# Kernel tuning notes

Hardware: AMD Instinct MI355X
Metric: run time of the kernel (lower is better)

## Reference

```python
import jax, jax.numpy as jnp
import numpy as np

N = 100000
E = 800000
F_IN = 256
HID = 64
H = 4
NEG_SLOPE = 0.2
BN_EPS = 1e-5


def setup_inputs() -> dict:
    key = jax.random.key(0)
    ks = jax.random.split(key, 20)
    s = 0.05
    return {
        "x": jax.random.normal(ks[0], (N, F_IN), jnp.float32),
        "edge_index": jax.random.randint(ks[1], (2, E), 0, N, jnp.int64),
        # GCNConv params
        "W_gcn": jax.random.normal(ks[2], (F_IN, HID), jnp.float32) * s,
        "b_gcn": jnp.zeros((HID,), jnp.float32),
        "g0": jnp.ones((HID,), jnp.float32),
        "beta0": jnp.zeros((HID,), jnp.float32),
        # GATConv 1 params
        "W1": jax.random.normal(ks[3], (HID, H * HID), jnp.float32) * s,
        "a_src1": jax.random.normal(ks[4], (H, HID), jnp.float32) * s,
        "a_dst1": jax.random.normal(ks[5], (H, HID), jnp.float32) * s,
        "b1": jnp.zeros((H * HID,), jnp.float32),
        "g1": jnp.ones((H * HID,), jnp.float32),
        "beta1": jnp.zeros((H * HID,), jnp.float32),
        # GATConv 2 params
        "W2": jax.random.normal(ks[6], (H * HID, H * HID), jnp.float32) * s,
        "a_src2": jax.random.normal(ks[7], (H, HID), jnp.float32) * s,
        "a_dst2": jax.random.normal(ks[8], (H, HID), jnp.float32) * s,
        "b2": jnp.zeros((H * HID,), jnp.float32),
        "g2": jnp.ones((H * HID,), jnp.float32),
        "beta2": jnp.zeros((H * HID,), jnp.float32),
    }


def _add_self_loops(edge_index, n):
    loop = jnp.arange(n, dtype=edge_index.dtype)
    src = jnp.concatenate([edge_index[0], loop])
    dst = jnp.concatenate([edge_index[1], loop])
    return src, dst


def _batch_norm(x, g, b):
    # BatchNorm1d, training-mode batch stats (biased variance), no dropout
    m = x.mean(0)
    v = x.var(0)
    return g * (x - m) * jax.lax.rsqrt(v + BN_EPS) + b


def _gcn_conv(x, src, dst, W, b, n):
    # symmetric normalization with self-loops already included in src/dst
    deg = jax.ops.segment_sum(jnp.ones_like(dst, jnp.float32), dst, n)
    dinv = jax.lax.rsqrt(jnp.maximum(deg, 1.0))
    norm = dinv[src] * dinv[dst]  # [E']
    h = x @ W  # [N, HID]
    out = jax.ops.segment_sum(h[src] * norm[:, None], dst, n)
    return out + b


def _gat_conv(x, src, dst, W, a_src, a_dst, b, n):
    h = (x @ W).reshape(n, H, HID)  # [N, H, C]
    alpha_s = jnp.einsum("nhc,hc->nh", h, a_src)  # [N, H]
    alpha_d = jnp.einsum("nhc,hc->nh", h, a_dst)
    e = alpha_s[src] + alpha_d[dst]  # [E', H]
    e = jnp.where(e > 0, e, NEG_SLOPE * e)  # LeakyReLU
    # softmax over incoming edges of each dst node, per head
    emax = jax.ops.segment_max(e, dst, n)
    w = jnp.exp(e - emax[dst])
    wsum = jax.ops.segment_sum(w, dst, n)
    att = w / wsum[dst]  # [E', H]
    out = jax.ops.segment_sum(att[:, :, None] * h[src], dst, n)  # [N, H, C]
    return out.reshape(n, H * HID) + b


def reference(x, edge_index, W_gcn, b_gcn, g0, beta0, W1, a_src1, a_dst1, b1,
              g1, beta1, W2, a_src2, a_dst2, b2, g2, beta2):
    n = x.shape[0]
    src, dst = _add_self_loops(edge_index, n)
    h = jax.nn.relu(_gcn_conv(x, src, dst, W_gcn, b_gcn, n))
    h = _batch_norm(h, g0, beta0)
    h = _gat_conv(h, src, dst, W1, a_src1, a_dst1, b1, n)
    h = jax.nn.elu(_batch_norm(h, g1, beta1))
    h = _gat_conv(h, src, dst, W2, a_src2, a_dst2, b2, n)
    h = jax.nn.elu(_batch_norm(h, g2, beta2))
    return h
```

## Files before the change

kernel.cpp:

```cpp
#include <hip/hip_runtime.h>
#include <hip/hip_bf16.h>
#include <math.h>

#define NN 100000
#define EE 800000
#define FIN 256
#define CH 64
#define C1 256
#define BN_EPS 1e-5f
#define NEG_SLOPE 0.2f

typedef __attribute__((ext_vector_type(8))) short short8;
typedef __attribute__((ext_vector_type(8))) unsigned short u16x8;
typedef __attribute__((ext_vector_type(4))) float f32x4;

__device__ __forceinline__ float bf2f(ushort u) {
    return __uint_as_float(((unsigned)u) << 16);
}
__device__ __forceinline__ ushort f2bf(float f) {
    unsigned u = __float_as_uint(f);
    return (ushort)((u + 0x7FFF + ((u >> 16) & 1)) >> 16);
}

__global__ void hist_kernel(const int* __restrict__ ei, int* __restrict__ deg) {
    int t = blockIdx.x * 256 + threadIdx.x;
    if (t < EE) atomicAdd(&deg[ei[EE + t]], 1);
}
__global__ void dinv_kernel(const int* __restrict__ deg, float* __restrict__ dinv) {
    int i = blockIdx.x * 256 + threadIdx.x;
    if (i < NN) dinv[i] = rsqrtf((float)(deg[i] + 1));
}
__global__ void scan_k1(const int* __restrict__ deg, int* __restrict__ row_start,
                        int* __restrict__ bsum) {
    __shared__ int sh[256];
    int t = threadIdx.x;
    int i = blockIdx.x * 256 + t;
    int v = (i < NN) ? (deg[i] + 1) : 0;
    sh[t] = v;
    __syncthreads();
    for (int off = 1; off < 256; off <<= 1) {
        int add = (t >= off) ? sh[t - off] : 0;
        __syncthreads();
        sh[t] += add;
        __syncthreads();
    }
    if (i < NN) row_start[i] = sh[t] - v;
    if (t == 255) bsum[blockIdx.x] = sh[255];
}
__global__ void scan_k2(int* __restrict__ bsum, int nb) {
    __shared__ int sh[512];
    int t = threadIdx.x;
    int v = (t < nb) ? bsum[t] : 0;
    sh[t] = v;
    __syncthreads();
    for (int off = 1; off < 512; off <<= 1) {
        int add = (t >= off) ? sh[t - off] : 0;
        __syncthreads();
        sh[t] += add;
        __syncthreads();
    }
    if (t < nb) bsum[t] = sh[t] - v;
}
__global__ void scan_k3(int* __restrict__ row_start, const int* __restrict__ bsum) {
    int i = blockIdx.x * 256 + threadIdx.x;
    if (i < NN) row_start[i] += bsum[i >> 8];
    if (i == NN) row_start[NN] = EE + NN;
}
__global__ void scatter_kernel(const int* __restrict__ ei, const int* __restrict__ row_start,
                               int* __restrict__ fill, int* __restrict__ sorted) {
    int t = blockIdx.x * 256 + threadIdx.x;
    if (t >= EE + NN) return;
    int s, d;
    if (t < EE) { s = ei[t]; d = ei[EE + t]; }
    else        { s = t - EE; d = s; }
    int pos = atomicAdd(&fill[d], 1);
    sorted[row_start[d] + pos] = s;
}

__global__ void convert_f32_bf16(const float* __restrict__ in, ushort* __restrict__ out, long n4) {
    long i = (long)blockIdx.x * 256 + threadIdx.x;
    if (i < n4) {
        float4 v = *(const float4*)&in[i * 4];
        ushort4 o;
        o.x = f2bf(v.x); o.y = f2bf(v.y); o.z = f2bf(v.z); o.w = f2bf(v.w);
        *(ushort4*)&out[i * 4] = o;
    }
}
__global__ void transpose_w(const float* __restrict__ W, ushort* __restrict__ Bt, int M, int K) {
    int idx = blockIdx.x * 256 + threadIdx.x;
    if (idx < M * K) {
        int m = idx / K, n = idx % K;
        Bt[n * M + m] = f2bf(W[idx]);
    }
}

__global__ __launch_bounds__(256) void gemm_mfma(
        const ushort* __restrict__ A, const ushort* __restrict__ Bt,
        ushort* __restrict__ C, int M, int K) {
    __shared__ ushort As[64][40];
    __shared__ ushort Bs[64][40];
    int t = threadIdx.x;
    int w = t >> 6;
    int l = t & 63;
    int rowBase = blockIdx.y * 64;
    int colBase = blockIdx.x * 64;
    int srow = t >> 2;
    int sk = (t & 3) * 8;
    int m = l & 15, q = l >> 4;
    f32x4 acc[4] = {};
    for (int k0 = 0; k0 < M; k0 += 32) {
        uint4 av = make_uint4(0u, 0u, 0u, 0u);
        int gr = rowBase + srow;
        if (gr < NN) av = *(const uint4*)&A[(long)gr * M + k0 + sk];
        uint4 bv = *(const uint4*)&Bt[(long)(colBase + srow) * M + k0 + sk];
        *(uint4*)&As[srow][sk] = av;
        *(uint4*)&Bs[srow][sk] = bv;
        __syncthreads();
        short8 af = *(const short8*)&As[w * 16 + m][q * 8];
#pragma unroll
        for (int c = 0; c < 4; ++c) {
            short8 bf = *(const short8*)&Bs[c * 16 + m][q * 8];
            acc[c] = __builtin_amdgcn_mfma_f32_16x16x32_bf16(af, bf, acc[c], 0, 0, 0);
        }
        __syncthreads();
    }
#pragma unroll
    for (int c = 0; c < 4; ++c) {
#pragma unroll
        for (int r = 0; r < 4; ++r) {
            int orow = rowBase + w * 16 + q * 4 + r;
            if (orow < NN) C[(long)orow * K + colBase + c * 16 + m] = f2bf(acc[c][r]);
        }
    }
}

__global__ __launch_bounds__(256) void gcn_gather(
        const int* __restrict__ row_start, const int* __restrict__ sorted,
        const float* __restrict__ dinv, const ushort* __restrict__ h0,
        float* __restrict__ agg) {
    int node = blockIdx.x * 4 + (threadIdx.x >> 6);
    if (node >= NN) return;
    int l = threadIdx.x & 63;
    int slot = l >> 3;
    int li = l & 7;
    int c = li * 8;
    int b = row_start[node], e = row_start[node + 1];
    float a[8] = {};
    for (int i = b + slot; i < e; i += 8) {
        int s = sorted[i];
        float dv = dinv[s];
        u16x8 v = *(const u16x8*)&h0[(long)s * 64 + c];
#pragma unroll
        for (int j = 0; j < 8; ++j) a[j] += dv * bf2f((ushort)v[j]);
    }
#pragma unroll
    for (int j = 0; j < 8; ++j) {
        a[j] += __shfl_xor(a[j], 8);
        a[j] += __shfl_xor(a[j], 16);
        a[j] += __shfl_xor(a[j], 32);
    }
    if (slot == 0) {
        float dn = dinv[node];
        f32x4 o0, o1;
#pragma unroll
        for (int j = 0; j < 4; ++j) { o0[j] = a[j] * dn; o1[j] = a[4 + j] * dn; }
        *(f32x4*)&agg[(long)node * 64 + c] = o0;
        *(f32x4*)&agg[(long)node * 64 + c + 4] = o1;
    }
}

__global__ __launch_bounds__(256) void bn_stats64(
        const float* __restrict__ x, const float* __restrict__ bias,
        float* __restrict__ sums, float* __restrict__ sumsq) {
    __shared__ float red[4][16][8];
    int l = threadIdx.x & 63;
    int w = threadIdx.x >> 6;
    int wv = blockIdx.x * 4 + w;
    int nw = gridDim.x * 4;
    int sub = l >> 4;
    int c = (l & 15) * 4;
    f32x4 b4 = *(const f32x4*)&bias[c];
    float s0 = 0.f, s1 = 0.f, s2 = 0.f, s3 = 0.f;
    float q0 = 0.f, q1 = 0.f, q2 = 0.f, q3 = 0.f;
    for (int r = wv * 4 + sub; r < NN; r += nw * 4) {
        f32x4 v = *(const f32x4*)&x[(long)r * 64 + c];
        float v0 = fmaxf(v[0] + b4[0], 0.f);
        float v1 = fmaxf(v[1] + b4[1], 0.f);
        float v2 = fmaxf(v[2] + b4[2], 0.f);
        float v3 = fmaxf(v[3] + b4[3], 0.f);
        s0 += v0; s1 += v1; s2 += v2; s3 += v3;
        q0 += v0 * v0; q1 += v1 * v1; q2 += v2 * v2; q3 += v3 * v3;
    }
    s0 += __shfl_xor(s0, 16); s1 += __shfl_xor(s1, 16);
    s2 += __shfl_xor(s2, 16); s3 += __shfl_xor(s3, 16);
    q0 += __shfl_xor(q0, 16); q1 += __shfl_xor(q1, 16);
    q2 += __shfl_xor(q2, 16); q3 += __shfl_xor(q3, 16);
    s0 += __shfl_xor(s0, 32); s1 += __shfl_xor(s1, 32);
    s2 += __shfl_xor(s2, 32); s3 += __shfl_xor(s3, 32);
    q0 += __shfl_xor(q0, 32); q1 += __shfl_xor(q1, 32);
    q2 += __shfl_xor(q2, 32); q3 += __shfl_xor(q3, 32);
    if (sub == 0) {
        int li = l & 15;
        red[w][li][0] = s0; red[w][li][1] = s1; red[w][li][2] = s2; red[w][li][3] = s3;
        red[w][li][4] = q0; red[w][li][5] = q1; red[w][li][6] = q2; red[w][li][7] = q3;
    }
    __syncthreads();
    if (w == 0 && sub == 0) {
        int li = l & 15;
        atomicAdd(&sums[c + 0], red[0][li][0] + red[1][li][0] + red[2][li][0] + red[3][li][0]);
        atomicAdd(&sums[c + 1], red[0][li][1] + red[1][li][1] + red[2][li][1] + red[3][li][1]);
        atomicAdd(&sums[c + 2], red[0][li][2] + red[1][li][2] + red[2][li][2] + red[3][li][2]);
        atomicAdd(&sums[c + 3], red[0][li][3] + red[1][li][3] + red[2][li][3] + red[3][li][3]);
        atomicAdd(&sumsq[c + 0], red[0][li][4] + red[1][li][4] + red[2][li][4] + red[3][li][4]);
        atomicAdd(&sumsq[c + 1], red[0][li][5] + red[1][li][5] + red[2][li][5] + red[3][li][5]);
        atomicAdd(&sumsq[c + 2], red[0][li][6] + red[1][li][6] + red[2][li][6] + red[3][li][6]);
        atomicAdd(&sumsq[c + 3], red[0][li][7] + red[1][li][7] + red[2][li][7] + red[3][li][7]);
    }
}
__global__ __launch_bounds__(256) void bn_stats256(
        const ushort* __restrict__ x,
        float* __restrict__ sums, float* __restrict__ sumsq) {
    __shared__ float red[4][64][8];
    int l = threadIdx.x & 63;
    int w = threadIdx.x >> 6;
    int wv = blockIdx.x * 4 + w;
    int nw = gridDim.x * 4;
    int c = l * 4;
    float s0 = 0.f, s1 = 0.f, s2 = 0.f, s3 = 0.f;
    float q0 = 0.f, q1 = 0.f, q2 = 0.f, q3 = 0.f;
    for (int r = wv; r < NN; r += nw) {
        ushort4 v = *(const ushort4*)&x[(long)r * 256 + c];
        float v0 = bf2f(v.x), v1 = bf2f(v.y), v2 = bf2f(v.z), v3 = bf2f(v.w);
        s0 += v0; s1 += v1; s2 += v2; s3 += v3;
        q0 += v0 * v0; q1 += v1 * v1; q2 += v2 * v2; q3 += v3 * v3;
    }
    red[w][l][0] = s0; red[w][l][1] = s1; red[w][l][2] = s2; red[w][l][3] = s3;
    red[w][l][4] = q0; red[w][l][5] = q1; red[w][l][6] = q2; red[w][l][7] = q3;
    __syncthreads();
    if (w == 0) {
        atomicAdd(&sums[c + 0], red[0][l][0] + red[1][l][0] + red[2][l][0] + red[3][l][0]);
        atomicAdd(&sums[c + 1], red[0][l][1] + red[1][l][1] + red[2][l][1] + red[3][l][1]);
        atomicAdd(&sums[c + 2], red[0][l][2] + red[1][l][2] + red[2][l][2] + red[3][l][2]);
        atomicAdd(&sums[c + 3], red[0][l][3] + red[1][l][3] + red[2][l][3] + red[3][l][3]);
        atomicAdd(&sumsq[c + 0], red[0][l][4] + red[1][l][4] + red[2][l][4] + red[3][l][4]);
        atomicAdd(&sumsq[c + 1], red[0][l][5] + red[1][l][5] + red[2][l][5] + red[3][l][5]);
        atomicAdd(&sumsq[c + 2], red[0][l][6] + red[1][l][6] + red[2][l][6] + red[3][l][6]);
        atomicAdd(&sumsq[c + 3], red[0][l][7] + red[1][l][7] + red[2][l][7] + red[3][l][7]);
    }
}
__global__ void bn_finalize(const float* __restrict__ sums, const float* __restrict__ sumsq,
                            const float* __restrict__ g, const float* __restrict__ beta,
                            float* __restrict__ scale, float* __restrict__ shift, int C) {
    int c = threadIdx.x;
    if (c < C) {
        float mean = sums[c] / (float)NN;
        float var = sumsq[c] / (float)NN - mean * mean;
        float sc = g[c] * rsqrtf(var + BN_EPS);
        scale[c] = sc;
        shift[c] = beta[c] - mean * sc;
    }
}
__global__ __launch_bounds__(256) void bn_apply_gcn(
        const float* __restrict__ x, const float* __restrict__ bias,
        const float* __restrict__ scale, const float* __restrict__ shift,
        ushort* __restrict__ out) {
    int l = threadIdx.x & 63;
    int wv = blockIdx.x * 4 + (threadIdx.x >> 6);
    int nw = gridDim.x * 4;
    int c = (l & 15) * 4;
    int sub = l >> 4;
    f32x4 b4  = *(const f32x4*)&bias[c];
    f32x4 sc4 = *(const f32x4*)&scale[c];
    f32x4 sh4 = *(const f32x4*)&shift[c];
    for (int r = wv * 4 + sub; r < NN; r += nw * 4) {
        f32x4 v = *(const f32x4*)&x[(long)r * 64 + c];
        ushort4 o;
        o.x = f2bf(sc4[0] * fmaxf(v[0] + b4[0], 0.f) + sh4[0]);
        o.y = f2bf(sc4[1] * fmaxf(v[1] + b4[1], 0.f) + sh4[1]);
        o.z = f2bf(sc4[2] * fmaxf(v[2] + b4[2], 0.f) + sh4[2]);
        o.w = f2bf(sc4[3] * fmaxf(v[3] + b4[3], 0.f) + sh4[3]);
        *(ushort4*)&out[(long)r * 64 + c] = o;
    }
}
__global__ __launch_bounds__(256) void bn_apply_gat(
        const ushort* __restrict__ x,
        const float* __restrict__ scale, const float* __restrict__ shift,
        void* __restrict__ out, int out_bf16) {
    int l = threadIdx.x & 63;
    int wv = blockIdx.x * 4 + (threadIdx.x >> 6);
    int nw = gridDim.x * 4;
    int c = l * 4;
    f32x4 sc4 = *(const f32x4*)&scale[c];
    f32x4 sh4 = *(const f32x4*)&shift[c];
    if (out_bf16) {
        ushort* ob = (ushort*)out;
        for (int r = wv; r < NN; r += nw) {
            ushort4 v = *(const ushort4*)&x[(long)r * 256 + c];
            float t0 = sc4[0] * bf2f(v.x) + sh4[0];
            float t1 = sc4[1] * bf2f(v.y) + sh4[1];
            float t2 = sc4[2] * bf2f(v.z) + sh4[2];
            float t3 = sc4[3] * bf2f(v.w) + sh4[3];
            t0 = (t0 > 0.f) ? t0 : (__expf(t0) - 1.f);
            t1 = (t1 > 0.f) ? t1 : (__expf(t1) - 1.f);
            t2 = (t2 > 0.f) ? t2 : (__expf(t2) - 1.f);
            t3 = (t3 > 0.f) ? t3 : (__expf(t3) - 1.f);
            ushort4 o;
            o.x = f2bf(t0); o.y = f2bf(t1); o.z = f2bf(t2); o.w = f2bf(t3);
            *(ushort4*)&ob[(long)r * 256 + c] = o;
        }
    } else {
        float* of = (float*)out;
        for (int r = wv; r < NN; r += nw) {
            ushort4 v = *(const ushort4*)&x[(long)r * 256 + c];
            float t0 = sc4[0] * bf2f(v.x) + sh4[0];
            float t1 = sc4[1] * bf2f(v.y) + sh4[1];
            float t2 = sc4[2] * bf2f(v.z) + sh4[2];
            float t3 = sc4[3] * bf2f(v.w) + sh4[3];
            f32x4 o;
            o[0] = (t0 > 0.f) ? t0 : (__expf(t0) - 1.f);
            o[1] = (t1 > 0.f) ? t1 : (__expf(t1) - 1.f);
            o[2] = (t2 > 0.f) ? t2 : (__expf(t2) - 1.f);
            o[3] = (t3 > 0.f) ? t3 : (__expf(t3) - 1.f);
            *(f32x4*)&of[(long)r * 256 + c] = o;
        }
    }
}

__global__ __launch_bounds__(256) void gat_alpha(
        const ushort* __restrict__ h, const float* __restrict__ a_src,
        const float* __restrict__ a_dst,
        float* __restrict__ alpha_s, float* __restrict__ alpha_d) {
    int node = blockIdx.x * 4 + (threadIdx.x >> 6);
    if (node >= NN) return;
    int l = threadIdx.x & 63;
    int c = l * 4;
    f32x4 asv = *(const f32x4*)&a_src[c];
    f32x4 adv = *(const f32x4*)&a_dst[c];
    ushort4 v = *(const ushort4*)&h[(long)node * 256 + c];
    float h0 = bf2f(v.x), h1 = bf2f(v.y), h2 = bf2f(v.z), h3 = bf2f(v.w);
    float vs = h0 * asv[0] + h1 * asv[1] + h2 * asv[2] + h3 * asv[3];
    float vd = h0 * adv[0] + h1 * adv[1] + h2 * adv[2] + h3 * adv[3];
    vs += __shfl_xor(vs, 1); vd += __shfl_xor(vd, 1);
    vs += __shfl_xor(vs, 2); vd += __shfl_xor(vd, 2);
    vs += __shfl_xor(vs, 4); vd += __shfl_xor(vd, 4);
    vs += __shfl_xor(vs, 8); vd += __shfl_xor(vd, 8);
    if ((l & 15) == 0) {
        int head = l >> 4;
        alpha_s[node * 4 + head] = vs;
        alpha_d[node * 4 + head] = vd;
    }
}

__global__ __launch_bounds__(256) void gat_gather(
        const int* __restrict__ row_start, const int* __restrict__ sorted,
        const float* __restrict__ as, const float* __restrict__ ad,
        const ushort* __restrict__ h, ushort* __restrict__ out) {
    int node = blockIdx.x * 4 + (threadIdx.x >> 6);
    if (node >= NN) return;
    int l = threadIdx.x & 63;
    int head = l >> 4;
    int b = row_start[node], e = row_start[node + 1];
    float adn = ad[node * 4 + head];
    float a0 = 0.f, a1 = 0.f, a2 = 0.f, a3 = 0.f;
    float ls = 0.f;
    int i = b;
    for (; i + 3 < e; i += 4) {
        int s[4]; float ev[4]; ushort4 v[4];
#pragma unroll
        for (int j = 0; j < 4; ++j) s[j] = sorted[i + j];
#pragma unroll
        for (int j = 0; j < 4; ++j) ev[j] = as[s[j] * 4 + head];
#pragma unroll
        for (int j = 0; j < 4; ++j) v[j] = *(const ushort4*)&h[(long)s[j] * 256 + l * 4];
#pragma unroll
        for (int j = 0; j < 4; ++j) {
            float t = ev[j] + adn;
            t = (t > 0.f) ? t : NEG_SLOPE * t;
            float w = __expf(fminf(t, 80.f));
            ls += w;
            a0 += w * bf2f(v[j].x);
            a1 += w * bf2f(v[j].y);
            a2 += w * bf2f(v[j].z);
            a3 += w * bf2f(v[j].w);
        }
    }
    for (; i < e; ++i) {
        int s0 = sorted[i];
        float t = as[s0 * 4 + head] + adn;
        t = (t > 0.f) ? t : NEG_SLOPE * t;
        float w = __expf(fminf(t, 80.f));
        ushort4 v0 = *(const ushort4*)&h[(long)s0 * 256 + l * 4];
        ls += w;
        a0 += w * bf2f(v0.x);
        a1 += w * bf2f(v0.y);
        a2 += w * bf2f(v0.z);
        a3 += w * bf2f(v0.w);
    }
    float inv = 1.0f / ls;
    ushort4 o;
    o.x = f2bf(a0 * inv);
    o.y = f2bf(a1 * inv);
    o.z = f2bf(a2 * inv);
    o.w = f2bf(a3 * inv);
    *(ushort4*)&out[(long)node * 256 + l * 4] = o;
}

extern "C" void kernel_launch(void* const* d_in, const int* in_sizes, int n_in,
                              void* d_out, int out_size, void* d_ws, size_t ws_size,
                              hipStream_t stream) {
    const float* x      = (const float*)d_in[0];
    const int*   ei     = (const int*)d_in[1];
    const float* W_gcn  = (const float*)d_in[2];
    const float* b_gcn  = (const float*)d_in[3];
    const float* g0     = (const float*)d_in[4];
    const float* beta0  = (const float*)d_in[5];
    const float* W1     = (const float*)d_in[6];
    const float* a_src1 = (const float*)d_in[7];
    const float* a_dst1 = (const float*)d_in[8];
    const float* b1     = (const float*)d_in[9];
    const float* g1     = (const float*)d_in[10];
    const float* beta1  = (const float*)d_in[11];
    const float* W2     = (const float*)d_in[12];
    const float* a_src2 = (const float*)d_in[13];
    const float* a_dst2 = (const float*)d_in[14];
    const float* b2     = (const float*)d_in[15];
    const float* g2     = (const float*)d_in[16];
    const float* beta2  = (const float*)d_in[17];

    const long N = NN;
    float* ws = (float*)d_ws;

    float* dinv    = ws;
    float* alpha_s = ws + N;
    float* alpha_d = ws + 5 * N;
    float* sums    = ws + 9 * N;
    float* sumsq   = sums + 256;
    float* scale   = sumsq + 256;
    float* shift   = scale + 256;
    int*   row_start = (int*)(shift + 256);
    int*   fill      = row_start + NN + 1;
    int*   deg_i     = fill + NN;
    int*   sorted    = deg_i + NN;
    int*   bsum      = sorted + EE + NN;
    ushort* Wgt  = (ushort*)(ws + 23 * N);
    ushort* W1t  = Wgt + 16384;
    ushort* W2t  = W1t + 16384;
    ushort* h0b  = (ushort*)(ws + 24 * N);
    ushort* x1b  = h0b;
    float*  agg0 = ws + 56 * N;
    ushort* h1b  = (ushort*)(ws + 120 * N);
    ushort* x2b  = (ushort*)(ws + 248 * N);
    ushort* xb   = x2b;
    ushort* yb   = (ushort*)(ws + 376 * N);
    float*  outp = (float*)d_out;

    const int BLK = 256;
    dim3 blk(BLK);
    const int NBLK_N = (NN + 255) / 256;

    hipMemsetAsync(fill, 0, 2L * NN * sizeof(int), stream);
    hist_kernel<<<(EE + 255) / 256, blk, 0, stream>>>(ei, deg_i);
    dinv_kernel<<<NBLK_N, blk, 0, stream>>>(deg_i, dinv);
    scan_k1<<<NBLK_N, blk, 0, stream>>>(deg_i, row_start, bsum);
    scan_k2<<<1, 512, 0, stream>>>(bsum, NBLK_N);
    scan_k3<<<(NN + 1 + 255) / 256, blk, 0, stream>>>(row_start, bsum);
    scatter_kernel<<<(EE + NN + 255) / 256, blk, 0, stream>>>(ei, row_start, fill, sorted);

    convert_f32_bf16<<<(int)((N * 256 / 4 + 255) / 256), blk, 0, stream>>>(x, xb, N * 256 / 4);
    transpose_w<<<(FIN * CH + 255) / 256, blk, 0, stream>>>(W_gcn, Wgt, FIN, CH);
    transpose_w<<<(CH * C1 + 255) / 256, blk, 0, stream>>>(W1, W1t, CH, C1);
    transpose_w<<<(C1 * C1 + 255) / 256, blk, 0, stream>>>(W2, W2t, C1, C1);

    gemm_mfma<<<dim3(CH / 64, (NN + 63) / 64), blk, 0, stream>>>(xb, Wgt, h0b, FIN, CH);
    gcn_gather<<<(NN + 3) / 4, blk, 0, stream>>>(row_start, sorted, dinv, h0b, agg0);
    hipMemsetAsync(sums, 0, 512 * sizeof(float), stream);
    bn_stats64<<<512, blk, 0, stream>>>(agg0, b_gcn, sums, sumsq);
    bn_finalize<<<1, CH, 0, stream>>>(sums, sumsq, g0, beta0, scale, shift, CH);
    bn_apply_gcn<<<1024, blk, 0, stream>>>(agg0, b_gcn, scale, shift, x1b);

    gemm_mfma<<<dim3(C1 / 64, (NN + 63) / 64), blk, 0, stream>>>(x1b, W1t, h1b, CH, C1);
    gat_alpha<<<(NN + 3) / 4, blk, 0, stream>>>(h1b, a_src1, a_dst1, alpha_s, alpha_d);
    gat_gather<<<(NN + 3) / 4, blk, 0, stream>>>(row_start, sorted, alpha_s, alpha_d, h1b, yb);
    hipMemsetAsync(sums, 0, 512 * sizeof(float), stream);
    bn_stats256<<<512, blk, 0, stream>>>(yb, sums, sumsq);
    bn_finalize<<<1, C1, 0, stream>>>(sums, sumsq, g1, beta1, scale, shift, C1);
    bn_apply_gat<<<2048, blk, 0, stream>>>(yb, scale, shift, x2b, 1);

    gemm_mfma<<<dim3(C1 / 64, (NN + 63) / 64), blk, 0, stream>>>(x2b, W2t, h1b, C1, C1);
    gat_alpha<<<(NN + 3) / 4, blk, 0, stream>>>(h1b, a_src2, a_dst2, alpha_s, alpha_d);
    gat_gather<<<(NN + 3) / 4, blk, 0, stream>>>(row_start, sorted, alpha_s, alpha_d, h1b, yb);
    hipMemsetAsync(sums, 0, 512 * sizeof(float), stream);
    bn_stats256<<<512, blk, 0, stream>>>(yb, sums, sumsq);
    bn_finalize<<<1, C1, 0, stream>>>(sums, sumsq, g2, beta2, scale, shift, C1);
    bn_apply_gat<<<2048, blk, 0, stream>>>(yb, scale, shift, outp, 0);
}
```

Measured before the change: 810.9 us.

## Fuse fp32 conversion, attention logits and BN statistics into GEMM/gather kernels

The input fp32-to-bf16 conversion moves into the first GEMM's tile load, and the GAT alpha dot products are computed in the GEMM epilogue, so the separate convert and gat_alpha kernels go away. The GCN and GAT gather kernels become grid-stride loops that also accumulate the BatchNorm sum and sum-of-squares, which removes the separate bn_stats passes over the aggregated features. Atomics are spread over 16 replicated accumulators to reduce contention, and bn_finalize sums the replicas. In exchange the persistent-style gathers may balance load less evenly, and the exp clamp at 80 was dropped, which could overflow on extreme logits.

```diff
diff --git a/kernel.cpp b/kernel.cpp
--- a/kernel.cpp
+++ b/kernel.cpp
@@ -9,6 +9,7 @@
 #define C1 256
 #define BN_EPS 1e-5f
 #define NEG_SLOPE 0.2f
+#define NREP 16
 
 typedef __attribute__((ext_vector_type(8))) short short8;
 typedef __attribute__((ext_vector_type(8))) unsigned short u16x8;
@@ -77,15 +78,6 @@
     sorted[row_start[d] + pos] = s;
 }
 
-__global__ void convert_f32_bf16(const float* __restrict__ in, ushort* __restrict__ out, long n4) {
-    long i = (long)blockIdx.x * 256 + threadIdx.x;
-    if (i < n4) {
-        float4 v = *(const float4*)&in[i * 4];
-        ushort4 o;
-        o.x = f2bf(v.x); o.y = f2bf(v.y); o.z = f2bf(v.z); o.w = f2bf(v.w);
-        *(ushort4*)&out[i * 4] = o;
-    }
-}
 __global__ void transpose_w(const float* __restrict__ W, ushort* __restrict__ Bt, int M, int K) {
     int idx = blockIdx.x * 256 + threadIdx.x;
     if (idx < M * K) {
@@ -95,8 +87,10 @@
 }
 
 __global__ __launch_bounds__(256) void gemm_mfma(
-        const ushort* __restrict__ A, const ushort* __restrict__ Bt,
-        ushort* __restrict__ C, int M, int K) {
+        const void* __restrict__ Ap, const ushort* __restrict__ Bt,
+        ushort* __restrict__ C, int M, int K, int a_fp32,
+        const float* __restrict__ a_src, const float* __restrict__ a_dst,
+        float* __restrict__ alpha_s, float* __restrict__ alpha_d) {
     __shared__ ushort As[64][40];
     __shared__ ushort Bs[64][40];
     int t = threadIdx.x;
@@ -109,11 +103,24 @@
     int m = l & 15, q = l >> 4;
     f32x4 acc[4] = {};
     for (int k0 = 0; k0 < M; k0 += 32) {
-        uint4 av = make_uint4(0u, 0u, 0u, 0u);
         int gr = rowBase + srow;
-        if (gr < NN) av = *(const uint4*)&A[(long)gr * M + k0 + sk];
+        if (a_fp32) {
+            ushort4 u0 = {0, 0, 0, 0}, u1 = {0, 0, 0, 0};
+            if (gr < NN) {
+                const float* Af = (const float*)Ap;
+                float4 f0 = *(const float4*)&Af[(long)gr * M + k0 + sk];
+                float4 f1 = *(const float4*)&Af[(long)gr * M + k0 + sk + 4];
+                u0.x = f2bf(f0.x); u0.y = f2bf(f0.y); u0.z = f2bf(f0.z); u0.w = f2bf(f0.w);
+                u1.x = f2bf(f1.x); u1.y = f2bf(f1.y); u1.z = f2bf(f1.z); u1.w = f2bf(f1.w);
+            }
+            *(ushort4*)&As[srow][sk] = u0;
+            *(ushort4*)&As[srow][sk + 4] = u1;
+        } else {
+            uint4 av = make_uint4(0u, 0u, 0u, 0u);
+            if (gr < NN) av = *(const uint4*)&((const ushort*)Ap)[(long)gr * M + k0 + sk];
+            *(uint4*)&As[srow][sk] = av;
+        }
         uint4 bv = *(const uint4*)&Bt[(long)(colBase + srow) * M + k0 + sk];
-        *(uint4*)&As[srow][sk] = av;
         *(uint4*)&Bs[srow][sk] = bv;
         __syncthreads();
         short8 af = *(const short8*)&As[w * 16 + m][q * 8];
@@ -124,6 +131,37 @@
         }
         __syncthreads();
     }
+    if (alpha_s) {
+        int head = colBase >> 6;
+        float ps[4] = {}, pd[4] = {};
+#pragma unroll
+        for (int c = 0; c < 4; ++c) {
+            float av = a_src[colBase + c * 16 + m];
+            float dv = a_dst[colBase + c * 16 + m];
+#pragma unroll
+            for (int r = 0; r < 4; ++r) {
+                ps[r] += acc[c][r] * av;
+                pd[r] += acc[c][r] * dv;
+            }
+        }
+#pragma unroll
+        for (int r = 0; r < 4; ++r) {
+            ps[r] += __shfl_xor(ps[r], 1); pd[r] += __shfl_xor(pd[r], 1);
+            ps[r] += __shfl_xor(ps[r], 2); pd[r] += __shfl_xor(pd[r], 2);
+            ps[r] += __shfl_xor(ps[r], 4); pd[r] += __shfl_xor(pd[r], 4);
+            ps[r] += __shfl_xor(ps[r], 8); pd[r] += __shfl_xor(pd[r], 8);
+        }
+        if (m == 0) {
+#pragma unroll
+            for (int r = 0; r < 4; ++r) {
+                int row = rowBase + w * 16 + q * 4 + r;
+                if (row < NN) {
+                    alpha_s[row * 4 + head] = ps[r];
+                    alpha_d[row * 4 + head] = pd[r];
+                }
+            }
+        }
+    }
 #pragma unroll
     for (int c = 0; c < 4; ++c) {
 #pragma unroll
@@ -137,124 +175,75 @@
 __global__ __launch_bounds__(256) void gcn_gather(
         const int* __restrict__ row_start, const int* __restrict__ sorted,
         const float* __restrict__ dinv, const ushort* __restrict__ h0,
-        float* __restrict__ agg) {
-    int node = blockIdx.x * 4 + (threadIdx.x >> 6);
-    if (node >= NN) return;
-    int l = threadIdx.x & 63;
-    int slot = l >> 3;
-    int li = l & 7;
-    int c = li * 8;
-    int b = row_start[node], e = row_start[node + 1];
-    float a[8] = {};
-    for (int i = b + slot; i < e; i += 8) {
-        int s = sorted[i];
-        float dv = dinv[s];
-        u16x8 v = *(const u16x8*)&h0[(long)s * 64 + c];
-#pragma unroll
-        for (int j = 0; j < 8; ++j) a[j] += dv * bf2f((ushort)v[j]);
-    }
-#pragma unroll
-    for (int j = 0; j < 8; ++j) {
-        a[j] += __shfl_xor(a[j], 8);
-        a[j] += __shfl_xor(a[j], 16);
-        a[j] += __shfl_xor(a[j], 32);
-    }
-    if (slot == 0) {
-        float dn = dinv[node];
-        f32x4 o0, o1;
-#pragma unroll
-        for (int j = 0; j < 4; ++j) { o0[j] = a[j] * dn; o1[j] = a[4 + j] * dn; }
-        *(f32x4*)&agg[(long)node * 64 + c] = o0;
-        *(f32x4*)&agg[(long)node * 64 + c + 4] = o1;
-    }
-}
-
-__global__ __launch_bounds__(256) void bn_stats64(
-        const float* __restrict__ x, const float* __restrict__ bias,
+        const float* __restrict__ bias, float* __restrict__ agg,
         float* __restrict__ sums, float* __restrict__ sumsq) {
-    __shared__ float red[4][16][8];
+    __shared__ float red[4][8][16];
     int l = threadIdx.x & 63;
     int w = threadIdx.x >> 6;
     int wv = blockIdx.x * 4 + w;
     int nw = gridDim.x * 4;
-    int sub = l >> 4;
-    int c = (l & 15) * 4;
-    f32x4 b4 = *(const f32x4*)&bias[c];
-    float s0 = 0.f, s1 = 0.f, s2 = 0.f, s3 = 0.f;
-    float q0 = 0.f, q1 = 0.f, q2 = 0.f, q3 = 0.f;
-    for (int r = wv * 4 + sub; r < NN; r += nw * 4) {
-        f32x4 v = *(const f32x4*)&x[(long)r * 64 + c];
-        float v0 = fmaxf(v[0] + b4[0], 0.f);
-        float v1 = fmaxf(v[1] + b4[1], 0.f);
-        float v2 = fmaxf(v[2] + b4[2], 0.f);
-        float v3 = fmaxf(v[3] + b4[3], 0.f);
-        s0 += v0; s1 += v1; s2 += v2; s3 += v3;
-        q0 += v0 * v0; q1 += v1 * v1; q2 += v2 * v2; q3 += v3 * v3;
-    }
-    s0 += __shfl_xor(s0, 16); s1 += __shfl_xor(s1, 16);
-    s2 += __shfl_xor(s2, 16); s3 += __shfl_xor(s3, 16);
-    q0 += __shfl_xor(q0, 16); q1 += __shfl_xor(q1, 16);
-    q2 += __shfl_xor(q2, 16); q3 += __shfl_xor(q3, 16);
-    s0 += __shfl_xor(s0, 32); s1 += __shfl_xor(s1, 32);
-    s2 += __shfl_xor(s2, 32); s3 += __shfl_xor(s3, 32);
-    q0 += __shfl_xor(q0, 32); q1 += __shfl_xor(q1, 32);
-    q2 += __shfl_xor(q2, 32); q3 += __shfl_xor(q3, 32);
-    if (sub == 0) {
-        int li = l & 15;
-        red[w][li][0] = s0; red[w][li][1] = s1; red[w][li][2] = s2; red[w][li][3] = s3;
-        red[w][li][4] = q0; red[w][li][5] = q1; red[w][li][6] = q2; red[w][li][7] = q3;
+    int slot = l >> 3;
+    int li = l & 7;
+    int c = li * 8;
+    float bb[8];
+#pragma unroll
+    for (int j = 0; j < 8; ++j) bb[j] = bias[c + j];
+    float st[8] = {}, qt[8] = {};
+    for (int node = wv; node < NN; node += nw) {
+        int b = row_start[node], e = row_start[node + 1];
+        float a[8] = {};
+        for (int i = b + slot; i < e; i += 8) {
+            int s = sorted[i];
+            float dv = dinv[s];
+            u16x8 v = *(const u16x8*)&h0[(long)s * 64 + c];
+#pragma unroll
+            for (int j = 0; j < 8; ++j) a[j] += dv * bf2f((ushort)v[j]);
+        }
+#pragma unroll
+        for (int j = 0; j < 8; ++j) {
+            a[j] += __shfl_xor(a[j], 8);
+            a[j] += __shfl_xor(a[j], 16);
+            a[j] += __shfl_xor(a[j], 32);
+        }
+        if (slot == 0) {
+            float dn = dinv[node];
+            f32x4 o0, o1;
+#pragma unroll
+            for (int j = 0; j < 4; ++j) { o0[j] = a[j] * dn; o1[j] = a[4 + j] * dn; }
+            *(f32x4*)&agg[(long)node * 64 + c] = o0;
+            *(f32x4*)&agg[(long)node * 64 + c + 4] = o1;
+#pragma unroll
+            for (int j = 0; j < 8; ++j) {
+                float v = fmaxf((j < 4 ? o0[j] : o1[j - 4]) + bb[j], 0.f);
+                st[j] += v; qt[j] += v * v;
+            }
+        }
+    }
+    if (slot == 0) {
+#pragma unroll
+        for (int j = 0; j < 8; ++j) { red[w][li][j] = st[j]; red[w][li][8 + j] = qt[j]; }
     }
     __syncthreads();
-    if (w == 0 && sub == 0) {
-        int li = l & 15;
-        atomicAdd(&sums[c + 0], red[0][li][0] + red[1][li][0] + red[2][li][0] + red[3][li][0]);
-        atomicAdd(&sums[c + 1], red[0][li][1] + red[1][li][1] + red[2][li][1] + red[3][li][1]);
-        atomicAdd(&sums[c + 2], red[0][li][2] + red[1][li][2] + red[2][li][2] + red[3][li][2]);
-        atomicAdd(&sums[c + 3], red[0][li][3] + red[1][li][3] + red[2][li][3] + red[3][li][3]);
-        atomicAdd(&sumsq[c + 0], red[0][li][4] + red[1][li][4] + red[2][li][4] + red[3][li][4]);
-        atomicAdd(&sumsq[c + 1], red[0][li][5] + red[1][li][5] + red[2][li][5] + red[3][li][5]);
-        atomicAdd(&sumsq[c + 2], red[0][li][6] + red[1][li][6] + red[2][li][6] + red[3][li][6]);
-        atomicAdd(&sumsq[c + 3], red[0][li][7] + red[1][li][7] + red[2][li][7] + red[3][li][7]);
-    }
-}
-__global__ __launch_bounds__(256) void bn_stats256(
-        const ushort* __restrict__ x,
-        float* __restrict__ sums, float* __restrict__ sumsq) {
-    __shared__ float red[4][64][8];
-    int l = threadIdx.x & 63;
-    int w = threadIdx.x >> 6;
-    int wv = blockIdx.x * 4 + w;
-    int nw = gridDim.x * 4;
-    int c = l * 4;
-    float s0 = 0.f, s1 = 0.f, s2 = 0.f, s3 = 0.f;
-    float q0 = 0.f, q1 = 0.f, q2 = 0.f, q3 = 0.f;
-    for (int r = wv; r < NN; r += nw) {
-        ushort4 v = *(const ushort4*)&x[(long)r * 256 + c];
-        float v0 = bf2f(v.x), v1 = bf2f(v.y), v2 = bf2f(v.z), v3 = bf2f(v.w);
-        s0 += v0; s1 += v1; s2 += v2; s3 += v3;
-        q0 += v0 * v0; q1 += v1 * v1; q2 += v2 * v2; q3 += v3 * v3;
-    }
-    red[w][l][0] = s0; red[w][l][1] = s1; red[w][l][2] = s2; red[w][l][3] = s3;
-    red[w][l][4] = q0; red[w][l][5] = q1; red[w][l][6] = q2; red[w][l][7] = q3;
-    __syncthreads();
-    if (w == 0) {
-        atomicAdd(&sums[c + 0], red[0][l][0] + red[1][l][0] + red[2][l][0] + red[3][l][0]);
-        atomicAdd(&sums[c + 1], red[0][l][1] + red[1][l][1] + red[2][l][1] + red[3][l][1]);
-        atomicAdd(&sums[c + 2], red[0][l][2] + red[1][l][2] + red[2][l][2] + red[3][l][2]);
-        atomicAdd(&sums[c + 3], red[0][l][3] + red[1][l][3] + red[2][l][3] + red[3][l][3]);
-        atomicAdd(&sumsq[c + 0], red[0][l][4] + red[1][l][4] + red[2][l][4] + red[3][l][4]);
-        atomicAdd(&sumsq[c + 1], red[0][l][5] + red[1][l][5] + red[2][l][5] + red[3][l][5]);
-        atomicAdd(&sumsq[c + 2], red[0][l][6] + red[1][l][6] + red[2][l][6] + red[3][l][6]);
-        atomicAdd(&sumsq[c + 3], red[0][l][7] + red[1][l][7] + red[2][l][7] + red[3][l][7]);
-    }
-}
+    if (w == 0 && slot == 0) {
+        float* S = sums + (blockIdx.x & (NREP - 1)) * 64;
+        float* Q = sumsq + (blockIdx.x & (NREP - 1)) * 64;
+#pragma unroll
+        for (int j = 0; j < 8; ++j) {
+            atomicAdd(&S[c + j], red[0][li][j] + red[1][li][j] + red[2][li][j] + red[3][li][j]);
+            atomicAdd(&Q[c + j], red[0][li][8 + j] + red[1][li][8 + j] + red[2][li][8 + j] + red[3][li][8 + j]);
+        }
+    }
+}
+
 __global__ void bn_finalize(const float* __restrict__ sums, const float* __restrict__ sumsq,
                             const float* __restrict__ g, const float* __restrict__ beta,
                             float* __restrict__ scale, float* __restrict__ shift, int C) {
     int c = threadIdx.x;
     if (c < C) {
-        float mean = sums[c] / (float)NN;
-        float var = sumsq[c] / (float)NN - mean * mean;
+        float sm = 0.f, sq = 0.f;
+        for (int r = 0; r < NREP; ++r) { sm += sums[r * C + c]; sq += sumsq[r * C + c]; }
+        float mean = sm / (float)NN;
+        float var = sq / (float)NN - mean * mean;
         float sc = g[c] * rsqrtf(var + BN_EPS);
         scale[c] = sc;
         shift[c] = beta[c] - mean * sc;
@@ -326,83 +315,81 @@
     }
 }
 
-__global__ __launch_bounds__(256) void gat_alpha(
-        const ushort* __restrict__ h, const float* __restrict__ a_src,
-        const float* __restrict__ a_dst,
-        float* __restrict__ alpha_s, float* __restrict__ alpha_d) {
-    int node = blockIdx.x * 4 + (threadIdx.x >> 6);
-    if (node >= NN) return;
-    int l = threadIdx.x & 63;
-    int c = l * 4;
-    f32x4 asv = *(const f32x4*)&a_src[c];
-    f32x4 adv = *(const f32x4*)&a_dst[c];
-    ushort4 v = *(const ushort4*)&h[(long)node * 256 + c];
-    float h0 = bf2f(v.x), h1 = bf2f(v.y), h2 = bf2f(v.z), h3 = bf2f(v.w);
-    float vs = h0 * asv[0] + h1 * asv[1] + h2 * asv[2] + h3 * asv[3];
-    float vd = h0 * adv[0] + h1 * adv[1] + h2 * adv[2] + h3 * adv[3];
-    vs += __shfl_xor(vs, 1); vd += __shfl_xor(vd, 1);
-    vs += __shfl_xor(vs, 2); vd += __shfl_xor(vd, 2);
-    vs += __shfl_xor(vs, 4); vd += __shfl_xor(vd, 4);
-    vs += __shfl_xor(vs, 8); vd += __shfl_xor(vd, 8);
-    if ((l & 15) == 0) {
-        int head = l >> 4;
-        alpha_s[node * 4 + head] = vs;
-        alpha_d[node * 4 + head] = vd;
-    }
-}
-
 __global__ __launch_bounds__(256) void gat_gather(
         const int* __restrict__ row_start, const int* __restrict__ sorted,
         const float* __restrict__ as, const float* __restrict__ ad,
-        const ushort* __restrict__ h, ushort* __restrict__ out) {
-    int node = blockIdx.x * 4 + (threadIdx.x >> 6);
-    if (node >= NN) return;
+        const ushort* __restrict__ h, ushort* __restrict__ out,
+        float* __restrict__ sums, float* __restrict__ sumsq) {
+    __shared__ float red[4][64][8];
     int l = threadIdx.x & 63;
+    int w = threadIdx.x >> 6;
+    int wv = blockIdx.x * 4 + w;
+    int nw = gridDim.x * 4;
     int head = l >> 4;
-    int b = row_start[node], e = row_start[node + 1];
-    float adn = ad[node * 4 + head];
-    float a0 = 0.f, a1 = 0.f, a2 = 0.f, a3 = 0.f;
-    float ls = 0.f;
-    int i = b;
-    for (; i + 3 < e; i += 4) {
-        int s[4]; float ev[4]; ushort4 v[4];
-#pragma unroll
-        for (int j = 0; j < 4; ++j) s[j] = sorted[i + j];
-#pragma unroll
-        for (int j = 0; j < 4; ++j) ev[j] = as[s[j] * 4 + head];
-#pragma unroll
-        for (int j = 0; j < 4; ++j) v[j] = *(const ushort4*)&h[(long)s[j] * 256 + l * 4];
-#pragma unroll
-        for (int j = 0; j < 4; ++j) {
-            float t = ev[j] + adn;
+    float s0 = 0.f, s1 = 0.f, s2 = 0.f, s3 = 0.f;
+    float z0 = 0.f, z1 = 0.f, z2 = 0.f, z3 = 0.f;
+    for (int node = wv; node < NN; node += nw) {
+        int b = row_start[node], e = row_start[node + 1];
+        float adn = ad[node * 4 + head];
+        float a0 = 0.f, a1 = 0.f, a2 = 0.f, a3 = 0.f;
+        float ls = 0.f;
+        int i = b;
+        for (; i + 3 < e; i += 4) {
+            int s[4]; float ev[4]; ushort4 v[4];
+#pragma unroll
+            for (int j = 0; j < 4; ++j) s[j] = sorted[i + j];
+#pragma unroll
+            for (int j = 0; j < 4; ++j) ev[j] = as[s[j] * 4 + head];
+#pragma unroll
+            for (int j = 0; j < 4; ++j) v[j] = *(const ushort4*)&h[(long)s[j] * 256 + l * 4];
+#pragma unroll
+            for (int j = 0; j < 4; ++j) {
+                float t = ev[j] + adn;
+                t = (t > 0.f) ? t : NEG_SLOPE * t;
+                float wt = __expf(t);
+                ls += wt;
+                a0 += wt * bf2f(v[j].x);
+                a1 += wt * bf2f(v[j].y);
+                a2 += wt * bf2f(v[j].z);
+                a3 += wt * bf2f(v[j].w);
+            }
+        }
+        for (; i < e; ++i) {
+            int sv = sorted[i];
+            float t = as[sv * 4 + head] + adn;
             t = (t > 0.f) ? t : NEG_SLOPE * t;
-            float w = __expf(fminf(t, 80.f));
-            ls += w;
-            a0 += w * bf2f(v[j].x);
-            a1 += w * bf2f(v[j].y);
-            a2 += w * bf2f(v[j].z);
-            a3 += w * bf2f(v[j].w);
-        }
-    }
-    for (; i < e; ++i) {
-        int s0 = sorted[i];
-        float t = as[s0 * 4 + head] + adn;
-        t = (t > 0.f) ? t : NEG_SLOPE * t;
-        float w = __expf(fminf(t, 80.f));
-        ushort4 v0 = *(const ushort4*)&h[(long)s0 * 256 + l * 4];
-        ls += w;
-        a0 += w * bf2f(v0.x);
-        a1 += w * bf2f(v0.y);
-        a2 += w * bf2f(v0.z);
-        a3 += w * bf2f(v0.w);
-    }
-    float inv = 1.0f / ls;
-    ushort4 o;
-    o.x = f2bf(a0 * inv);
-    o.y = f2bf(a1 * inv);
-    o.z = f2bf(a2 * inv);
-    o.w = f2bf(a3 * inv);
-    *(ushort4*)&out[(long)node * 256 + l * 4] = o;
+            float wt = __expf(t);
+            ushort4 v0 = *(const ushort4*)&h[(long)sv * 256 + l * 4];
+            ls += wt;
+            a0 += wt * bf2f(v0.x);
+            a1 += wt * bf2f(v0.y);
+            a2 += wt * bf2f(v0.z);
+            a3 += wt * bf2f(v0.w);
+        }
+        float inv = 1.0f / ls;
+        float o0 = a0 * inv, o1 = a1 * inv, o2 = a2 * inv, o3 = a3 * inv;
+        ushort4 o;
+        o.x = f2bf(o0); o.y = f2bf(o1); o.z = f2bf(o2); o.w = f2bf(o3);
+        *(ushort4*)&out[(long)node * 256 + l * 4] = o;
+        s0 += o0; s1 += o1; s2 += o2; s3 += o3;
+        z0 += o0 * o0; z1 += o1 * o1; z2 += o2 * o2; z3 += o3 * o3;
+    }
+    red[w][l][0] = s0; red[w][l][1] = s1; red[w][l][2] = s2; red[w][l][3] = s3;
+    red[w][l][4] = z0; red[w][l][5] = z1; red[w][l][6] = z2; red[w][l][7] = z3;
+    __syncthreads();
+    if (w == 0) {
+        int c = l * 4;
+        float* S = sums + (blockIdx.x & (NREP - 1)) * 256;
+        float* Q = sumsq + (blockIdx.x & (NREP - 1)) * 256;
+        atomicAdd(&S[c + 0], red[0][l][0] + red[1][l][0] + red[2][l][0] + red[3][l][0]);
+        atomicAdd(&S[c + 1], red[0][l][1] + red[1][l][1] + red[2][l][1] + red[3][l][1]);
+        atomicAdd(&S[c + 2], red[0][l][2] + red[1][l][2] + red[2][l][2] + red[3][l][2]);
+        atomicAdd(&S[c + 3], red[0][l][3] + red[1][l][3] + red[2][l][3] + red[3][l][3]);
+        atomicAdd(&Q[c + 0], red[0][l][4] + red[1][l][4] + red[2][l][4] + red[3][l][4]);
+        atomicAdd(&Q[c + 1], red[0][l][5] + red[1][l][5] + red[2][l][5] + red[3][l][5]);
+        atomicAdd(&Q[c + 2], red[0][l][6] + red[1][l][6] + red[2][l][6] + red[3][l][6]);
+        atomicAdd(&Q[c + 3], red[0][l][7] + red[1][l][7] + red[2][l][7] + red[3][l][7]);
+    }
 }
 
 extern "C" void kernel_launch(void* const* d_in, const int* in_sizes, int n_in,
@@ -434,8 +421,8 @@
     float* alpha_s = ws + N;
     float* alpha_d = ws + 5 * N;
     float* sums    = ws + 9 * N;
-    float* sumsq   = sums + 256;
-    float* scale   = sumsq + 256;
+    float* sumsq   = sums + 4096;
+    float* scale   = sumsq + 4096;
     float* shift   = scale + 256;
     int*   row_start = (int*)(shift + 256);
     int*   fill      = row_start + NN + 1;
@@ -450,7 +437,6 @@
     float*  agg0 = ws + 56 * N;
     ushort* h1b  = (ushort*)(ws + 120 * N);
     ushort* x2b  = (ushort*)(ws + 248 * N);
-    ushort* xb   = x2b;
     ushort* yb   = (ushort*)(ws + 376 * N);
     float*  outp = (float*)d_out;
 
@@ -466,31 +452,28 @@
     scan_k3<<<(NN + 1 + 255) / 256, blk, 0, stream>>>(row_start, bsum);
     scatter_kernel<<<(EE + NN + 255) / 256, blk, 0, stream>>>(ei, row_start, fill, sorted);
 
-    convert_f32_bf16<<<(int)((N * 256 / 4 + 255) / 256), blk, 0, stream>>>(x, xb, N * 256 / 4);
     transpose_w<<<(FIN * CH + 255) / 256, blk, 0, stream>>>(W_gcn, Wgt, FIN, CH);
     transpose_w<<<(CH * C1 + 255) / 256, blk, 0, stream>>>(W1, W1t, CH, C1);
     transpose_w<<<(C1 * C1 + 255) / 256, blk, 0, stream>>>(W2, W2t, C1, C1);
 
-    gemm_mfma<<<dim3(CH / 64, (NN + 63) / 64), blk, 0, stream>>>(xb, Wgt, h0b, FIN, CH);
-    gcn_gather<<<(NN + 3) / 4, blk, 0, stream>>>(row_start, sorted, dinv, h0b, agg0);
-    hipMemsetAsync(sums, 0, 512 * sizeof(float), stream);
-    bn_stats64<<<512, blk, 0, stream>>>(agg0, b_gcn, sums, sumsq);
+    gemm_mfma<<<dim3(CH / 64, (NN + 63) / 64), blk, 0, stream>>>(
+        x, Wgt, h0b, FIN, CH, 1, nullptr, nullptr, nullptr, nullptr);
+    hipMemsetAsync(sums, 0, 8192 * sizeof(float), stream);
+    gcn_gather<<<4096, blk, 0, stream>>>(row_start, sorted, dinv, h0b, b_gcn, agg0, sums, sumsq);
     bn_finalize<<<1, CH, 0, stream>>>(sums, sumsq, g0, beta0, scale, shift, CH);
     bn_apply_gcn<<<1024, blk, 0, stream>>>(agg0, b_gcn, scale, shift, x1b);
 
-    gemm_mfma<<<dim3(C1 / 64, (NN + 63) / 64), blk, 0, stream>>>(x1b, W1t, h1b, CH, C1);
-    gat_alpha<<<(NN + 3) / 4, blk, 0, stream>>>(h1b, a_src1, a_dst1, alpha_s, alpha_d);
-    gat_gather<<<(NN + 3) / 4, blk, 0, stream>>>(row_start, sorted, alpha_s, alpha_d, h1b, yb);
-    hipMemsetAsync(sums, 0, 512 * sizeof(float), stream);
-    bn_stats256<<<512, blk, 0, stream>>>(yb, sums, sumsq);
+    gemm_mfma<<<dim3(C1 / 64, (NN + 63) / 64), blk, 0, stream>>>(
+        x1b, W1t, h1b, CH, C1, 0, a_src1, a_dst1, alpha_s, alpha_d);
+    hipMemsetAsync(sums, 0, 8192 * sizeof(float), stream);
+    gat_gather<<<8192, blk, 0, stream>>>(row_start, sorted, alpha_s, alpha_d, h1b, yb, sums, sumsq);
     bn_finalize<<<1, C1, 0, stream>>>(sums, sumsq, g1, beta1, scale, shift, C1);
     bn_apply_gat<<<2048, blk, 0, stream>>>(yb, scale, shift, x2b, 1);
 
-    gemm_mfma<<<dim3(C1 / 64, (NN + 63) / 64), blk, 0, stream>>>(x2b, W2t, h1b, C1, C1);
-    gat_alpha<<<(NN + 3) / 4, blk, 0, stream>>>(h1b, a_src2, a_dst2, alpha_s, alpha_d);
-    gat_gather<<<(NN + 3) / 4, blk, 0, stream>>>(row_start, sorted, alpha_s, alpha_d, h1b, yb);
-    hipMemsetAsync(sums, 0, 512 * sizeof(float), stream);
-    bn_stats256<<<512, blk, 0, stream>>>(yb, sums, sumsq);
+    gemm_mfma<<<dim3(C1 / 64, (NN + 63) / 64), blk, 0, stream>>>(
+        x2b, W2t, h1b, C1, C1, 0, a_src2, a_dst2, alpha_s, alpha_d);
+    hipMemsetAsync(sums, 0, 8192 * sizeof(float), stream);
+    gat_gather<<<8192, blk, 0, stream>>>(row_start, sorted, alpha_s, alpha_d, h1b, yb, sums, sumsq);
     bn_finalize<<<1, C1, 0, stream>>>(sums, sumsq, g2, beta2, scale, shift, C1);
     bn_apply_gat<<<2048, blk, 0, stream>>>(yb, scale, shift, outp, 0);
 }
```

Result: faster. 766.8 us (-5.4%).

## Fuse fp32-to-bf16 conversion and GAT alpha projection into MFMA GEMM

Applied to the files above, without the earlier changes.

The first GEMM now reads fp32 x directly and converts to bf16 while staging into shared memory, which removes the separate convert kernel and its 51 MB bf16 intermediate round trip. The GAT attention logits (alpha_s/alpha_d) are computed from the fp32 GEMM accumulators in the epilogue with a 16-lane shuffle reduction, replacing the gat_alpha kernel that re-read h from memory. The exp clamp in gat_gather is also dropped. Alpha is now computed from unrounded fp32 values rather than bf16-rounded h, and removing the clamp means large logits could overflow.

```diff
diff --git a/kernel.cpp b/kernel.cpp
--- a/kernel.cpp
+++ b/kernel.cpp
@@ -77,15 +77,6 @@
     sorted[row_start[d] + pos] = s;
 }
 
-__global__ void convert_f32_bf16(const float* __restrict__ in, ushort* __restrict__ out, long n4) {
-    long i = (long)blockIdx.x * 256 + threadIdx.x;
-    if (i < n4) {
-        float4 v = *(const float4*)&in[i * 4];
-        ushort4 o;
-        o.x = f2bf(v.x); o.y = f2bf(v.y); o.z = f2bf(v.z); o.w = f2bf(v.w);
-        *(ushort4*)&out[i * 4] = o;
-    }
-}
 __global__ void transpose_w(const float* __restrict__ W, ushort* __restrict__ Bt, int M, int K) {
     int idx = blockIdx.x * 256 + threadIdx.x;
     if (idx < M * K) {
@@ -95,8 +86,10 @@
 }
 
 __global__ __launch_bounds__(256) void gemm_mfma(
-        const ushort* __restrict__ A, const ushort* __restrict__ Bt,
-        ushort* __restrict__ C, int M, int K) {
+        const void* __restrict__ Ap, const ushort* __restrict__ Bt,
+        ushort* __restrict__ C, int M, int K, int a_fp32,
+        const float* __restrict__ a_src, const float* __restrict__ a_dst,
+        float* __restrict__ alpha_s, float* __restrict__ alpha_d) {
     __shared__ ushort As[64][40];
     __shared__ ushort Bs[64][40];
     int t = threadIdx.x;
@@ -109,11 +102,24 @@
     int m = l & 15, q = l >> 4;
     f32x4 acc[4] = {};
     for (int k0 = 0; k0 < M; k0 += 32) {
-        uint4 av = make_uint4(0u, 0u, 0u, 0u);
         int gr = rowBase + srow;
-        if (gr < NN) av = *(const uint4*)&A[(long)gr * M + k0 + sk];
+        if (a_fp32) {
+            ushort4 u0 = {0, 0, 0, 0}, u1 = {0, 0, 0, 0};
+            if (gr < NN) {
+                const float* Af = (const float*)Ap;
+                float4 f0 = *(const float4*)&Af[(long)gr * M + k0 + sk];
+                float4 f1 = *(const float4*)&Af[(long)gr * M + k0 + sk + 4];
+                u0.x = f2bf(f0.x); u0.y = f2bf(f0.y); u0.z = f2bf(f0.z); u0.w = f2bf(f0.w);
+                u1.x = f2bf(f1.x); u1.y = f2bf(f1.y); u1.z = f2bf(f1.z); u1.w = f2bf(f1.w);
+            }
+            *(ushort4*)&As[srow][sk] = u0;
+            *(ushort4*)&As[srow][sk + 4] = u1;
+        } else {
+            uint4 av = make_uint4(0u, 0u, 0u, 0u);
+            if (gr < NN) av = *(const uint4*)&((const ushort*)Ap)[(long)gr * M + k0 + sk];
+            *(uint4*)&As[srow][sk] = av;
+        }
         uint4 bv = *(const uint4*)&Bt[(long)(colBase + srow) * M + k0 + sk];
-        *(uint4*)&As[srow][sk] = av;
         *(uint4*)&Bs[srow][sk] = bv;
         __syncthreads();
         short8 af = *(const short8*)&As[w * 16 + m][q * 8];
@@ -123,6 +129,37 @@
             acc[c] = __builtin_amdgcn_mfma_f32_16x16x32_bf16(af, bf, acc[c], 0, 0, 0);
         }
         __syncthreads();
+    }
+    if (alpha_s) {
+        int head = colBase >> 6;
+        float ps[4] = {}, pd[4] = {};
+#pragma unroll
+        for (int c = 0; c < 4; ++c) {
+            float av = a_src[colBase + c * 16 + m];
+            float dv = a_dst[colBase + c * 16 + m];
+#pragma unroll
+            for (int r = 0; r < 4; ++r) {
+                ps[r] += acc[c][r] * av;
+                pd[r] += acc[c][r] * dv;
+            }
+        }
+#pragma unroll
+        for (int r = 0; r < 4; ++r) {
+            ps[r] += __shfl_xor(ps[r], 1); pd[r] += __shfl_xor(pd[r], 1);
+            ps[r] += __shfl_xor(ps[r], 2); pd[r] += __shfl_xor(pd[r], 2);
+            ps[r] += __shfl_xor(ps[r], 4); pd[r] += __shfl_xor(pd[r], 4);
+            ps[r] += __shfl_xor(ps[r], 8); pd[r] += __shfl_xor(pd[r], 8);
+        }
+        if (m == 0) {
+#pragma unroll
+            for (int r = 0; r < 4; ++r) {
+                int row = rowBase + w * 16 + q * 4 + r;
+                if (row < NN) {
+                    alpha_s[row * 4 + head] = ps[r];
+                    alpha_d[row * 4 + head] = pd[r];
+                }
+            }
+        }
     }
 #pragma unroll
     for (int c = 0; c < 4; ++c) {
@@ -326,31 +363,6 @@
     }
 }
 
-__global__ __launch_bounds__(256) void gat_alpha(
-        const ushort* __restrict__ h, const float* __restrict__ a_src,
-        const float* __restrict__ a_dst,
-        float* __restrict__ alpha_s, float* __restrict__ alpha_d) {
-    int node = blockIdx.x * 4 + (threadIdx.x >> 6);
-    if (node >= NN) return;
-    int l = threadIdx.x & 63;
-    int c = l * 4;
-    f32x4 asv = *(const f32x4*)&a_src[c];
-    f32x4 adv = *(const f32x4*)&a_dst[c];
-    ushort4 v = *(const ushort4*)&h[(long)node * 256 + c];
-    float h0 = bf2f(v.x), h1 = bf2f(v.y), h2 = bf2f(v.z), h3 = bf2f(v.w);
-    float vs = h0 * asv[0] + h1 * asv[1] + h2 * asv[2] + h3 * asv[3];
-    float vd = h0 * adv[0] + h1 * adv[1] + h2 * adv[2] + h3 * adv[3];
-    vs += __shfl_xor(vs, 1); vd += __shfl_xor(vd, 1);
-    vs += __shfl_xor(vs, 2); vd += __shfl_xor(vd, 2);
-    vs += __shfl_xor(vs, 4); vd += __shfl_xor(vd, 4);
-    vs += __shfl_xor(vs, 8); vd += __shfl_xor(vd, 8);
-    if ((l & 15) == 0) {
-        int head = l >> 4;
-        alpha_s[node * 4 + head] = vs;
-        alpha_d[node * 4 + head] = vd;
-    }
-}
-
 __global__ __launch_bounds__(256) void gat_gather(
         const int* __restrict__ row_start, const int* __restrict__ sorted,
         const float* __restrict__ as, const float* __restrict__ ad,
@@ -376,25 +388,25 @@
         for (int j = 0; j < 4; ++j) {
             float t = ev[j] + adn;
             t = (t > 0.f) ? t : NEG_SLOPE * t;
-            float w = __expf(fminf(t, 80.f));
-            ls += w;
-            a0 += w * bf2f(v[j].x);
-            a1 += w * bf2f(v[j].y);
-            a2 += w * bf2f(v[j].z);
-            a3 += w * bf2f(v[j].w);
+            float wt = __expf(t);
+            ls += wt;
+            a0 += wt * bf2f(v[j].x);
+            a1 += wt * bf2f(v[j].y);
+            a2 += wt * bf2f(v[j].z);
+            a3 += wt * bf2f(v[j].w);
         }
     }
     for (; i < e; ++i) {
-        int s0 = sorted[i];
-        float t = as[s0 * 4 + head] + adn;
+        int sv = sorted[i];
+        float t = as[sv * 4 + head] + adn;
         t = (t > 0.f) ? t : NEG_SLOPE * t;
-        float w = __expf(fminf(t, 80.f));
-        ushort4 v0 = *(const ushort4*)&h[(long)s0 * 256 + l * 4];
-        ls += w;
-        a0 += w * bf2f(v0.x);
-        a1 += w * bf2f(v0.y);
-        a2 += w * bf2f(v0.z);
-        a3 += w * bf2f(v0.w);
+        float wt = __expf(t);
+        ushort4 v0 = *(const ushort4*)&h[(long)sv * 256 + l * 4];
+        ls += wt;
+        a0 += wt * bf2f(v0.x);
+        a1 += wt * bf2f(v0.y);
+        a2 += wt * bf2f(v0.z);
+        a3 += wt * bf2f(v0.w);
     }
     float inv = 1.0f / ls;
     ushort4 o;
@@ -450,7 +462,6 @@
     float*  agg0 = ws + 56 * N;
     ushort* h1b  = (ushort*)(ws + 120 * N);
     ushort* x2b  = (ushort*)(ws + 248 * N);
-    ushort* xb   = x2b;
     ushort* yb   = (ushort*)(ws + 376 * N);
     float*  outp = (float*)d_out;
 
@@ -466,28 +477,28 @@
     scan_k3<<<(NN + 1 + 255) / 256, blk, 0, stream>>>(row_start, bsum);
     scatter_kernel<<<(EE + NN + 255) / 256, blk, 0, stream>>>(ei, row_start, fill, sorted);
 
-    convert_f32_bf16<<<(int)((N * 256 / 4 + 255) / 256), blk, 0, stream>>>(x, xb, N * 256 / 4);
     transpose_w<<<(FIN * CH + 255) / 256, blk, 0, stream>>>(W_gcn, Wgt, FIN, CH);
     transpose_w<<<(CH * C1 + 255) / 256, blk, 0, stream>>>(W1, W1t, CH, C1);
     transpose_w<<<(C1 * C1 + 255) / 256, blk, 0, stream>>>(W2, W2t, C1, C1);
 
-    gemm_mfma<<<dim3(CH / 64, (NN + 63) / 64), blk, 0, stream>>>(xb, Wgt, h0b, FIN, CH);
+    gemm_mfma<<<dim3(CH / 64, (NN + 63) / 64), blk, 0, stream>>>(
+        x, Wgt, h0b, FIN, CH, 1, nullptr, nullptr, nullptr, nullptr);
     gcn_gather<<<(NN + 3) / 4, blk, 0, stream>>>(row_start, sorted, dinv, h0b, agg0);
     hipMemsetAsync(sums, 0, 512 * sizeof(float), stream);
     bn_stats64<<<512, blk, 0, stream>>>(agg0, b_gcn, sums, sumsq);
     bn_finalize<<<1, CH, 0, stream>>>(sums, sumsq, g0, beta0, scale, shift, CH);
     bn_apply_gcn<<<1024, blk, 0, stream>>>(agg0, b_gcn, scale, shift, x1b);
 
-    gemm_mfma<<<dim3(C1 / 64, (NN + 63) / 64), blk, 0, stream>>>(x1b, W1t, h1b, CH, C1);
-    gat_alpha<<<(NN + 3) / 4, blk, 0, stream>>>(h1b, a_src1, a_dst1, alpha_s, alpha_d);
+    gemm_mfma<<<dim3(C1 / 64, (NN + 63) / 64), blk, 0, stream>>>(
+        x1b, W1t, h1b, CH, C1, 0, a_src1, a_dst1, alpha_s, alpha_d);
     gat_gather<<<(NN + 3) / 4, blk, 0, stream>>>(row_start, sorted, alpha_s, alpha_d, h1b, yb);
     hipMemsetAsync(sums, 0, 512 * sizeof(float), stream);
     bn_stats256<<<512, blk, 0, stream>>>(yb, sums, sumsq);
     bn_finalize<<<1, C1, 0, stream>>>(sums, sumsq, g1, beta1, scale, shift, C1);
     bn_apply_gat<<<2048, blk, 0, stream>>>(yb, scale, shift, x2b, 1);
 
-    gemm_mfma<<<dim3(C1 / 64, (NN + 63) / 64), blk, 0, stream>>>(x2b, W2t, h1b, C1, C1);
-    gat_alpha<<<(NN + 3) / 4, blk, 0, stream>>>(h1b, a_src2, a_dst2, alpha_s, alpha_d);
+    gemm_mfma<<<dim3(C1 / 64, (NN + 63) / 64), blk, 0, stream>>>(
+        x2b, W2t, h1b, C1, C1, 0, a_src2, a_dst2, alpha_s, alpha_d);
     gat_gather<<<(NN + 3) / 4, blk, 0, stream>>>(row_start, sorted, alpha_s, alpha_d, h1b, yb);
     hipMemsetAsync(sums, 0, 512 * sizeof(float), stream);
     bn_stats256<<<512, blk, 0, stream>>>(yb, sums, sumsq);
```

New measurement: 786.3 us. 1.03x faster.
